# Kernel optimization log

Hardware: AMD Instinct MI355X
Metric: run time of the kernel (lower is better)

The kernel has to match this reference:

```python
import jax, jax.numpy as jnp
import numpy as np
import math

B, S, D = 1, 4096, 2048
H, KVH, HD = 32, 8, 64
W = 512            # sliding window size (== block size)
THETA = 10000.0
EPS = 1e-5
INTER = 5632
PRE_SCALE = 1.0 / math.sqrt(2.0)


def setup_inputs() -> dict:
    key = jax.random.key(0)
    ks = jax.random.split(key, 8)
    def w(k, shape, fan_in):
        return jax.random.normal(k, shape, jnp.float32) * (fan_in ** -0.5)
    return {
        "hidden_states": jax.random.normal(ks[0], (B, S, D), jnp.float32),
        "mixer_norm_w": jnp.ones((D,), jnp.float32),
        "wq": w(ks[1], (D, H * HD), D),
        "wk": w(ks[2], (D, KVH * HD), D),
        "wv": w(ks[3], (D, KVH * HD), D),
        "wo": w(ks[4], (H * HD, D), H * HD),
        "mlp_norm_w": jnp.ones((D,), jnp.float32),
        "w_gate": w(ks[5], (D, 2 * INTER), D),
        "w_down": w(ks[6], (INTER, D), INTER),
    }


def rmsnorm(x, w, eps=EPS):
    return x * jax.lax.rsqrt(jnp.mean(x * x, axis=-1, keepdims=True) + eps) * w


def rope(x):
    # x: [B, S, h, HD]; rotate-half RoPE
    half = HD // 2
    inv_freq = 1.0 / (THETA ** (jnp.arange(0, HD, 2, dtype=jnp.float32) / HD))
    freqs = jnp.arange(S, dtype=jnp.float32)[:, None] * inv_freq[None, :]  # [S, half]
    cos = jnp.cos(freqs)[None, :, None, :]
    sin = jnp.sin(freqs)[None, :, None, :]
    x1, x2 = x[..., :half], x[..., half:]
    return jnp.concatenate([x1 * cos - x2 * sin, x2 * cos + x1 * sin], axis=-1)


def sliding_attention(x, wq, wk, wv, wo):
    # x already pre-scaled; returns attn output (pre /pre_scale)
    q = (x @ wq).reshape(B, S, H, HD)
    k = (x @ wk).reshape(B, S, KVH, HD)
    v = (x @ wv).reshape(B, S, KVH, HD)
    q, k = rope(q), rope(k)
    rep = H // KVH
    k = jnp.repeat(k, rep, axis=2)  # [B,S,H,HD]
    v = jnp.repeat(v, rep, axis=2)
    nb = S // W
    qb = q.reshape(B, nb, W, H, HD)
    kb = k.reshape(B, nb, W, H, HD)
    vb = v.reshape(B, nb, W, H, HD)
    zeros = jnp.zeros((B, 1, W, H, HD), q.dtype)
    kw = jnp.concatenate([jnp.concatenate([zeros, kb[:, :-1]], axis=1), kb], axis=2)  # [B,nb,2W,H,HD]
    vw = jnp.concatenate([jnp.concatenate([zeros, vb[:, :-1]], axis=1), vb], axis=2)
    # local mask [nb, W, 2W]
    blk = jnp.arange(nb)[:, None, None]
    q_pos = blk * W + jnp.arange(W)[None, :, None]
    k_pos = blk * W - W + jnp.arange(2 * W)[None, None, :]
    mask = (k_pos >= 0) & (k_pos <= q_pos) & (q_pos - k_pos < W)
    scores = jnp.einsum("bnqhd,bnkhd->bhnqk", qb, kw) * (HD ** -0.5)
    scores = jnp.where(mask[None, None], scores, jnp.finfo(scores.dtype).min)
    p = jax.nn.softmax(scores, axis=-1)
    out = jnp.einsum("bhnqk,bnkhd->bnqhd", p, vw).reshape(B, S, H * HD)
    return out @ wo


def reference(hidden_states, mixer_norm_w, wq, wk, wv, wo, mlp_norm_w, w_gate, w_down):
    residual = hidden_states
    x = rmsnorm(hidden_states, mixer_norm_w)
    attn_out = sliding_attention(x * PRE_SCALE, wq, wk, wv, wo) / PRE_SCALE
    h = residual + attn_out
    xn = rmsnorm(h, mlp_norm_w)
    gv = xn @ w_gate
    gate, y = gv[..., :INTER], gv[..., INTER:]
    mlp_out = (jax.nn.silu(gate) * y) @ w_down
    return h + mlp_out
```

## Files before the change

kernel.cpp:

```cpp
#include <hip/hip_runtime.h>
#include <stdint.h>

typedef __attribute__((ext_vector_type(8))) short s16x8;
typedef __attribute__((ext_vector_type(4))) float f32x4;

#define GLD_LDS16(gp, lp) __builtin_amdgcn_global_load_lds( \
    (__attribute__((address_space(1))) void*)(void*)(gp), \
    (__attribute__((address_space(3))) void*)(lp), 16, 0, 0)

__device__ __forceinline__ float b2f(unsigned short s) {
    unsigned int u = ((unsigned int)s) << 16;
    return __builtin_bit_cast(float, u);
}
__device__ __forceinline__ unsigned short f2b(float f) {
    unsigned int u = __builtin_bit_cast(unsigned int, f);
    u = (u + 0x7FFFu + ((u >> 16) & 1u)) >> 16;
    return (unsigned short)u;
}
__device__ __forceinline__ f32x4 mfma16(s16x8 a, s16x8 b, f32x4 c) {
    return __builtin_amdgcn_mfma_f32_16x16x32_bf16(a, b, c, 0, 0, 0);
}
template <int N> __device__ __forceinline__ void waitvm() {
    if constexpr (N == 3) asm volatile("s_waitcnt vmcnt(3)" ::: "memory");
    else if constexpr (N == 4) asm volatile("s_waitcnt vmcnt(4)" ::: "memory");
}

__global__ __launch_bounds__(256) void rmsnorm_bf16(
    const float* __restrict__ x, const float* __restrict__ wgt,
    unsigned short* __restrict__ out)
{
    const int row = blockIdx.x;
    const int t = threadIdx.x;
    const float* xr = x + (size_t)row * 2048;
    float4 a = *(const float4*)(xr + t * 8);
    float4 b = *(const float4*)(xr + t * 8 + 4);
    float ss = a.x*a.x + a.y*a.y + a.z*a.z + a.w*a.w
             + b.x*b.x + b.y*b.y + b.z*b.z + b.w*b.w;
    #pragma unroll
    for (int d = 1; d < 64; d <<= 1) ss += __shfl_xor(ss, d);
    __shared__ float red[4];
    if ((t & 63) == 0) red[t >> 6] = ss;
    __syncthreads();
    float tot = red[0] + red[1] + red[2] + red[3];
    float inv = rsqrtf(tot * (1.0f / 2048.0f) + 1e-5f);
    float vals[8] = {a.x, a.y, a.z, a.w, b.x, b.y, b.z, b.w};
    const float* wr_ = wgt + t * 8;
    s16x8 ov;
    #pragma unroll
    for (int j = 0; j < 8; ++j) ov[j] = (short)f2b(vals[j] * inv * wr_[j]);
    *(s16x8*)(out + (size_t)row * 2048 + t * 8) = ov;
}

__global__ __launch_bounds__(256) void transpose_to_bf16(
    const float* __restrict__ in, unsigned short* __restrict__ out, int K, int N)
{
    __shared__ float tile[64][65];
    const int n0 = blockIdx.x * 64, k0 = blockIdx.y * 64;
    const int t = threadIdx.x;
    const int kr = t >> 4, nc = (t & 15) * 4;
    #pragma unroll
    for (int i = 0; i < 4; ++i) {
        float4 v = *(const float4*)(in + (size_t)(k0 + kr + i * 16) * N + n0 + nc);
        tile[nc + 0][kr + i * 16] = v.x;
        tile[nc + 1][kr + i * 16] = v.y;
        tile[nc + 2][kr + i * 16] = v.z;
        tile[nc + 3][kr + i * 16] = v.w;
    }
    __syncthreads();
    const int nr = t >> 3, kc = (t & 7) * 8;
    #pragma unroll
    for (int p = 0; p < 2; ++p) {
        s16x8 o;
        #pragma unroll
        for (int j = 0; j < 8; ++j) o[j] = (short)f2b(tile[nr + p * 32][kc + j]);
        *(s16x8*)(out + (size_t)(n0 + nr + p * 32) * K + k0 + kc) = o;
    }
}

template <int BN, int EPI>
__global__ __launch_bounds__(512, 2) void gemmq(
    const unsigned short* __restrict__ A,
    const unsigned short* __restrict__ B,
    void* __restrict__ Cv,
    const float* __restrict__ ADD,
    int N, int K)
{
    constexpr int WN  = BN / 4;
    constexpr int HN  = WN / 2;
    constexpr int NJQ = WN / 32;
    constexpr int NBU = BN / 64;
    constexpr int ABUF = 256 * 64;
    constexpr int BBUF = BN * 64;
    constexpr int W1   = 4;
    constexpr int W2   = (BN == 256) ? 4 : 3;
    constexpr int WEND = (BN == 256) ? 4 : 3;
    __shared__ __align__(16) unsigned short As[2 * ABUF];
    __shared__ __align__(16) unsigned short Bs[2 * BBUF];

    const int t = threadIdx.x;
    const int l = t & 63, w = t >> 6;
    const int l15 = l & 15, lg = l >> 4;
    const int wr = w >> 2, wc = w & 3;
    const int x7 = l15 & 7;
    const int cc0 = ((lg) ^ x7) << 3;
    const int cc1 = ((4 | lg) ^ x7) << 3;

    const int nwg = (int)gridDim.x;
    const int orig = (int)blockIdx.x;
    const int q8 = nwg >> 3, r8 = nwg & 7;
    const int xcd = orig & 7, lid = orig >> 3;
    const int wg = (xcd < r8 ? xcd * (q8 + 1) : r8 * (q8 + 1) + (xcd - r8) * q8) + lid;
    const int m0 = (wg & 15) * 256;
    const int n0 = (wg >> 4) * BN;

    const int tr = t >> 3;
    const int scol = ((t & 7) ^ (tr & 7)) << 3;
    const unsigned short* pA[4];
    #pragma unroll
    for (int u = 0; u < 4; ++u) {
        const int lrow = u * 64 + tr;
        const int g = ((lrow >> 6) & 1) * 128 + (lrow >> 7) * 64 + (lrow & 63);
        pA[u] = A + (size_t)(m0 + g) * K + scol;
    }
    const unsigned short* pB[NBU];
    #pragma unroll
    for (int u = 0; u < NBU; ++u) {
        const int lrow = u * 64 + tr;
        const int h = lrow / (BN / 2), rem = lrow % (BN / 2);
        const int g = (rem / HN) * WN + h * HN + (rem % HN);
        pB[u] = B + (size_t)(n0 + g) * K + scol;
    }

    f32x4 acc[2][2][4][NJQ] = {};
    s16x8 aF[4][2];
    s16x8 bF[2][NJQ][2];

    const int NT = K / 64;

    GLD_LDS16(pA[0], &As[0 * 4096 + t * 8]);
    GLD_LDS16(pA[1], &As[1 * 4096 + t * 8]);
    #pragma unroll
    for (int u = 0; u < NBU; ++u) GLD_LDS16(pB[u], &Bs[u * 4096 + t * 8]);
    GLD_LDS16(pA[2], &As[2 * 4096 + t * 8]);
    GLD_LDS16(pA[3], &As[3 * 4096 + t * 8]);
    waitvm<WEND>();
    __builtin_amdgcn_s_barrier();

    for (int kt = 0; kt < NT; ++kt) {
        const int rb  = (kt & 1) ? ABUF : 0;
        const int rbB = (kt & 1) ? BBUF : 0;
        const int wb  = ABUF - rb;
        const int wbB = BBUF - rbB;
        const int knext = (kt + 1 < NT ? kt + 1 : kt) * 64;

        #pragma unroll
        for (int i = 0; i < 4; ++i) {
            const int lr = wr * 64 + i * 16 + l15;
            aF[i][0] = *(const s16x8*)&As[rb + lr * 64 + cc0];
            aF[i][1] = *(const s16x8*)&As[rb + lr * 64 + cc1];
        }
        #pragma unroll
        for (int j = 0; j < NJQ; ++j) {
            const int lr = wc * HN + j * 16 + l15;
            bF[0][j][0] = *(const s16x8*)&Bs[rbB + lr * 64 + cc0];
            bF[0][j][1] = *(const s16x8*)&Bs[rbB + lr * 64 + cc1];
        }
        GLD_LDS16(pA[0] + knext, &As[wb + 0 * 4096 + t * 8]);
        GLD_LDS16(pA[1] + knext, &As[wb + 1 * 4096 + t * 8]);
        __builtin_amdgcn_s_barrier();
        __builtin_amdgcn_s_setprio(1);
        #pragma unroll
        for (int kk = 0; kk < 2; ++kk)
            #pragma unroll
            for (int i = 0; i < 4; ++i)
                #pragma unroll
                for (int j = 0; j < NJQ; ++j)
                    acc[0][0][i][j] = mfma16(aF[i][kk], bF[0][j][kk], acc[0][0][i][j]);
        __builtin_amdgcn_s_setprio(0);
        waitvm<W1>();
        __builtin_amdgcn_s_barrier();

        #pragma unroll
        for (int j = 0; j < NJQ; ++j) {
            const int lr = (BN / 2) + wc * HN + j * 16 + l15;
            bF[1][j][0] = *(const s16x8*)&Bs[rbB + lr * 64 + cc0];
            bF[1][j][1] = *(const s16x8*)&Bs[rbB + lr * 64 + cc1];
        }
        #pragma unroll
        for (int u = 0; u < NBU / 2; ++u)
            GLD_LDS16(pB[u] + knext, &Bs[wbB + u * 4096 + t * 8]);
        __builtin_amdgcn_s_barrier();
        __builtin_amdgcn_s_setprio(1);
        #pragma unroll
        for (int kk = 0; kk < 2; ++kk)
            #pragma unroll
            for (int i = 0; i < 4; ++i)
                #pragma unroll
                for (int j = 0; j < NJQ; ++j)
                    acc[0][1][i][j] = mfma16(aF[i][kk], bF[1][j][kk], acc[0][1][i][j]);
        __builtin_amdgcn_s_setprio(0);
        waitvm<W2>();
        __builtin_amdgcn_s_barrier();

        #pragma unroll
        for (int i = 0; i < 4; ++i) {
            const int lr = 128 + wr * 64 + i * 16 + l15;
            aF[i][0] = *(const s16x8*)&As[rb + lr * 64 + cc0];
            aF[i][1] = *(const s16x8*)&As[rb + lr * 64 + cc1];
        }
        #pragma unroll
        for (int u = NBU / 2; u < NBU; ++u)
            GLD_LDS16(pB[u] + knext, &Bs[wbB + u * 4096 + t * 8]);
        __builtin_amdgcn_s_barrier();
        __builtin_amdgcn_s_setprio(1);
        #pragma unroll
        for (int kk = 0; kk < 2; ++kk)
            #pragma unroll
            for (int i = 0; i < 4; ++i)
                #pragma unroll
                for (int j = 0; j < NJQ; ++j)
                    acc[1][0][i][j] = mfma16(aF[i][kk], bF[0][j][kk], acc[1][0][i][j]);
        __builtin_amdgcn_s_setprio(0);
        __builtin_amdgcn_s_barrier();

        GLD_LDS16(pA[2] + knext, &As[wb + 2 * 4096 + t * 8]);
        GLD_LDS16(pA[3] + knext, &As[wb + 3 * 4096 + t * 8]);
        __builtin_amdgcn_s_barrier();
        __builtin_amdgcn_s_setprio(1);
        #pragma unroll
        for (int kk = 0; kk < 2; ++kk)
            #pragma unroll
            for (int i = 0; i < 4; ++i)
                #pragma unroll
                for (int j = 0; j < NJQ; ++j)
                    acc[1][1][i][j] = mfma16(aF[i][kk], bF[1][j][kk], acc[1][1][i][j]);
        __builtin_amdgcn_s_setprio(0);
        waitvm<WEND>();
        __builtin_amdgcn_s_barrier();
    }

    #pragma unroll
    for (int qm = 0; qm < 2; ++qm)
        #pragma unroll
        for (int i = 0; i < 4; ++i)
            #pragma unroll
            for (int r = 0; r < 4; ++r) {
                const int row = m0 + wr * 128 + qm * 64 + i * 16 + lg * 4 + r;
                const size_t rbase = (size_t)row * N;
                #pragma unroll
                for (int qn = 0; qn < 2; ++qn)
                    #pragma unroll
                    for (int j = 0; j < NJQ; ++j) {
                        const int col = n0 + wc * WN + qn * HN + j * 16 + l15;
                        float v = acc[qm][qn][i][j][r];
                        if constexpr (EPI == 0) {
                            ((unsigned short*)Cv)[rbase + col] = f2b(v);
                        } else {
                            ((float*)Cv)[rbase + col] = v + ADD[rbase + col];
                        }
                    }
            }
}

__global__ __launch_bounds__(512, 2) void gemm_glu(
    const unsigned short* __restrict__ A,
    const unsigned short* __restrict__ Bg,
    const unsigned short* __restrict__ By,
    unsigned short* __restrict__ act,
    int N, int K)
{
    constexpr int ABUF = 256 * 64, BBUF = 128 * 64;
    __shared__ __align__(16) unsigned short As[2 * ABUF];
    __shared__ __align__(16) unsigned short Bgs[2 * BBUF];
    __shared__ __align__(16) unsigned short Bys[2 * BBUF];

    const int t = threadIdx.x;
    const int l = t & 63, w = t >> 6;
    const int l15 = l & 15, lg = l >> 4;
    const int wr = w >> 2, wc = w & 3;
    const int x7 = l15 & 7;
    const int cc0 = ((lg) ^ x7) << 3;
    const int cc1 = ((4 | lg) ^ x7) << 3;

    const int nwg = (int)gridDim.x;
    const int orig = (int)blockIdx.x;
    const int q8 = nwg >> 3;
    const int xcd = orig & 7, lid = orig >> 3;
    const int wg = xcd * q8 + lid;
    const int m0 = (wg & 15) * 256;
    const int n0 = (wg >> 4) * 128;

    const int tr = t >> 3;
    const int scol = ((t & 7) ^ (tr & 7)) << 3;
    const unsigned short* pA[4];
    #pragma unroll
    for (int u = 0; u < 4; ++u) {
        const int lrow = u * 64 + tr;
        const int g = ((lrow >> 6) & 1) * 128 + (lrow >> 7) * 64 + (lrow & 63);
        pA[u] = A + (size_t)(m0 + g) * K + scol;
    }
    const unsigned short *pG[2], *pY[2];
    #pragma unroll
    for (int u = 0; u < 2; ++u) {
        const int g = (tr >> 4) * 32 + u * 16 + (tr & 15);
        pG[u] = Bg + (size_t)(n0 + g) * K + scol;
        pY[u] = By + (size_t)(n0 + g) * K + scol;
    }

    f32x4 accG[2][2][4] = {};
    f32x4 accY[2][2][4] = {};
    s16x8 aF[4][2];
    s16x8 gF[2][2], yF[2][2];

    const int NT = K / 64;

    GLD_LDS16(pA[0], &As[0 * 4096 + t * 8]);
    GLD_LDS16(pA[1], &As[1 * 4096 + t * 8]);
    GLD_LDS16(pG[0], &Bgs[0 * 4096 + t * 8]);
    GLD_LDS16(pY[0], &Bys[0 * 4096 + t * 8]);
    GLD_LDS16(pG[1], &Bgs[1 * 4096 + t * 8]);
    GLD_LDS16(pY[1], &Bys[1 * 4096 + t * 8]);
    GLD_LDS16(pA[2], &As[2 * 4096 + t * 8]);
    GLD_LDS16(pA[3], &As[3 * 4096 + t * 8]);
    waitvm<4>();
    __builtin_amdgcn_s_barrier();

    for (int kt = 0; kt < NT; ++kt) {
        const int rb  = (kt & 1) ? ABUF : 0;
        const int rbB = (kt & 1) ? BBUF : 0;
        const int wb  = ABUF - rb;
        const int wbB = BBUF - rbB;
        const int knext = (kt + 1 < NT ? kt + 1 : kt) * 64;

        #pragma unroll
        for (int i = 0; i < 4; ++i) {
            const int lr = wr * 64 + i * 16 + l15;
            aF[i][0] = *(const s16x8*)&As[rb + lr * 64 + cc0];
            aF[i][1] = *(const s16x8*)&As[rb + lr * 64 + cc1];
        }
        {
            const int lr = wc * 16 + l15;
            gF[0][0] = *(const s16x8*)&Bgs[rbB + lr * 64 + cc0];
            gF[0][1] = *(const s16x8*)&Bgs[rbB + lr * 64 + cc1];
            yF[0][0] = *(const s16x8*)&Bys[rbB + lr * 64 + cc0];
            yF[0][1] = *(const s16x8*)&Bys[rbB + lr * 64 + cc1];
        }
        GLD_LDS16(pA[0] + knext, &As[wb + 0 * 4096 + t * 8]);
        GLD_LDS16(pA[1] + knext, &As[wb + 1 * 4096 + t * 8]);
        __builtin_amdgcn_s_barrier();
        __builtin_amdgcn_s_setprio(1);
        #pragma unroll
        for (int kk = 0; kk < 2; ++kk)
            #pragma unroll
            for (int i = 0; i < 4; ++i) {
                accG[0][0][i] = mfma16(aF[i][kk], gF[0][kk], accG[0][0][i]);
                accY[0][0][i] = mfma16(aF[i][kk], yF[0][kk], accY[0][0][i]);
            }
        __builtin_amdgcn_s_setprio(0);
        waitvm<4>();
        __builtin_amdgcn_s_barrier();

        {
            const int lr = 64 + wc * 16 + l15;
            gF[1][0] = *(const s16x8*)&Bgs[rbB + lr * 64 + cc0];
            gF[1][1] = *(const s16x8*)&Bgs[rbB + lr * 64 + cc1];
            yF[1][0] = *(const s16x8*)&Bys[rbB + lr * 64 + cc0];
            yF[1][1] = *(const s16x8*)&Bys[rbB + lr * 64 + cc1];
        }
        GLD_LDS16(pG[0] + knext, &Bgs[wbB + 0 * 4096 + t * 8]);
        GLD_LDS16(pY[0] + knext, &Bys[wbB + 0 * 4096 + t * 8]);
        __builtin_amdgcn_s_barrier();
        __builtin_amdgcn_s_setprio(1);
        #pragma unroll
        for (int kk = 0; kk < 2; ++kk)
            #pragma unroll
            for (int i = 0; i < 4; ++i) {
                accG[0][1][i] = mfma16(aF[i][kk], gF[1][kk], accG[0][1][i]);
                accY[0][1][i] = mfma16(aF[i][kk], yF[1][kk], accY[0][1][i]);
            }
        __builtin_amdgcn_s_setprio(0);
        waitvm<4>();
        __builtin_amdgcn_s_barrier();

        #pragma unroll
        for (int i = 0; i < 4; ++i) {
            const int lr = 128 + wr * 64 + i * 16 + l15;
            aF[i][0] = *(const s16x8*)&As[rb + lr * 64 + cc0];
            aF[i][1] = *(const s16x8*)&As[rb + lr * 64 + cc1];
        }
        GLD_LDS16(pG[1] + knext, &Bgs[wbB + 1 * 4096 + t * 8]);
        GLD_LDS16(pY[1] + knext, &Bys[wbB + 1 * 4096 + t * 8]);
        __builtin_amdgcn_s_barrier();
        __builtin_amdgcn_s_setprio(1);
        #pragma unroll
        for (int kk = 0; kk < 2; ++kk)
            #pragma unroll
            for (int i = 0; i < 4; ++i) {
                accG[1][0][i] = mfma16(aF[i][kk], gF[0][kk], accG[1][0][i]);
                accY[1][0][i] = mfma16(aF[i][kk], yF[0][kk], accY[1][0][i]);
            }
        __builtin_amdgcn_s_setprio(0);
        __builtin_amdgcn_s_barrier();

        GLD_LDS16(pA[2] + knext, &As[wb + 2 * 4096 + t * 8]);
        GLD_LDS16(pA[3] + knext, &As[wb + 3 * 4096 + t * 8]);
        __builtin_amdgcn_s_barrier();
        __builtin_amdgcn_s_setprio(1);
        #pragma unroll
        for (int kk = 0; kk < 2; ++kk)
            #pragma unroll
            for (int i = 0; i < 4; ++i) {
                accG[1][1][i] = mfma16(aF[i][kk], gF[1][kk], accG[1][1][i]);
                accY[1][1][i] = mfma16(aF[i][kk], yF[1][kk], accY[1][1][i]);
            }
        __builtin_amdgcn_s_setprio(0);
        waitvm<4>();
        __builtin_amdgcn_s_barrier();
    }

    #pragma unroll
    for (int qm = 0; qm < 2; ++qm)
        #pragma unroll
        for (int i = 0; i < 4; ++i)
            #pragma unroll
            for (int r = 0; r < 4; ++r) {
                const int row = m0 + wr * 128 + qm * 64 + i * 16 + lg * 4 + r;
                const size_t rbase = (size_t)row * N;
                #pragma unroll
                for (int qn = 0; qn < 2; ++qn) {
                    const int col = n0 + wc * 32 + qn * 16 + l15;
                    float g = accG[qm][qn][i][r];
                    float y = accY[qm][qn][i][r];
                    float sg = g / (1.0f + expf(-g));
                    act[rbase + col] = f2b(sg * y);
                }
            }
}

__global__ void rope_tab_k(float2* __restrict__ tab) {
    int i = blockIdx.x * 256 + threadIdx.x;
    if (i >= 4096 * 32) return;
    int s = i >> 5, d = i & 31;
    float inv = exp2f(-(float)d * (13.287712379549449f / 32.0f));
    float fr = (float)s * inv;
    float sv, cv;
    sincosf(fr, &sv, &cv);
    tab[i] = make_float2(cv, sv);
}

__global__ void rope_apply_k(unsigned short* __restrict__ qkv, const float2* __restrict__ tab) {
    int i = blockIdx.x * 256 + threadIdx.x;
    if (i >= 4096 * 40 * 4) return;
    int dg = i & 3;
    int rest = i >> 2;
    int head = rest % 40;
    int s = rest / 40;
    int off = head < 32 ? head * 64 : 2048 + (head - 32) * 64;
    unsigned short* p = qkv + (size_t)s * 3072 + off + dg * 8;
    s16x8 x1 = *(const s16x8*)p;
    s16x8 x2 = *(const s16x8*)(p + 32);
    const float2* tb = tab + s * 32 + dg * 8;
    s16x8 o1, o2;
    #pragma unroll
    for (int j = 0; j < 8; ++j) {
        float2 cs = tb[j];
        float a = b2f((unsigned short)x1[j]);
        float b = b2f((unsigned short)x2[j]);
        o1[j] = (short)f2b(a * cs.x - b * cs.y);
        o2[j] = (short)f2b(b * cs.x + a * cs.y);
    }
    *(s16x8*)p = o1;
    *(s16x8*)(p + 32) = o2;
}

__global__ __launch_bounds__(256) void attn_swa(
    const unsigned short* __restrict__ qkv,
    unsigned short* __restrict__ out)
{
    constexpr int LDQ = 3072;
    const int qb = blockIdx.x;
    const int h = blockIdx.y;
    const int kvh = h >> 2;
    const int q0 = qb * 64;
    const int t = threadIdx.x, l = t & 63, w = t >> 6;
    const int l15 = l & 15, lg = l >> 4;

    __shared__ unsigned short Kl[64 * 64];
    __shared__ unsigned short Vt[64 * 72];
    __shared__ unsigned short Pl[4 * 16 * 72];

    s16x8 qf[2];
    {
        const unsigned short* qp = qkv + (size_t)(q0 + w * 16 + l15) * LDQ + h * 64 + lg * 8;
        qf[0] = *(const s16x8*)(qp);
        qf[1] = *(const s16x8*)(qp + 32);
    }
    float m_run[4] = {-1e30f, -1e30f, -1e30f, -1e30f};
    float l_run[4] = {0.f, 0.f, 0.f, 0.f};
    f32x4 o[4] = {};

    const float SC = 0.0625f * 1.4426950408889634f;
    const int kt_lo = qb >= 8 ? qb - 8 : 0;

    for (int kt = kt_lo; kt <= qb; ++kt) {
        const int ks = kt * 64;
        __syncthreads();
        {
            const unsigned short* kg = qkv + (size_t)(ks + (t >> 3)) * LDQ + 2048 + kvh * 64 + (t & 7) * 8;
            GLD_LDS16(kg, Kl + t * 8);
            GLD_LDS16(kg + (size_t)32 * LDQ, Kl + t * 8 + 2048);
        }
        {
            const unsigned short* vg = qkv + (size_t)(ks + l) * LDQ + 2560 + kvh * 64 + w * 16;
            s16x8 v0 = *(const s16x8*)vg;
            s16x8 v1 = *(const s16x8*)(vg + 8);
            #pragma unroll
            for (int j = 0; j < 8; ++j) Vt[(w * 16 + j) * 72 + l] = (unsigned short)v0[j];
            #pragma unroll
            for (int j = 0; j < 8; ++j) Vt[(w * 16 + 8 + j) * 72 + l] = (unsigned short)v1[j];
        }
        __syncthreads();

        f32x4 sf[4] = {};
        #pragma unroll
        for (int kf = 0; kf < 4; ++kf) {
            #pragma unroll
            for (int kk = 0; kk < 2; ++kk) {
                s16x8 kb = *(const s16x8*)(Kl + (kf * 16 + l15) * 64 + kk * 32 + lg * 8);
                sf[kf] = mfma16(qf[kk], kb, sf[kf]);
            }
        }

        float tmax[4];
        #pragma unroll
        for (int r = 0; r < 4; ++r) {
            int qrow = q0 + w * 16 + lg * 4 + r;
            float mx = -1e30f;
            #pragma unroll
            for (int kf = 0; kf < 4; ++kf) {
                int key = ks + kf * 16 + l15;
                bool valid = (key <= qrow) && (qrow - key < 512);
                if (valid) mx = fmaxf(mx, sf[kf][r]);
            }
            #pragma unroll
            for (int d2 = 1; d2 < 16; d2 <<= 1) mx = fmaxf(mx, __shfl_xor(mx, d2));
            tmax[r] = mx;
        }

        float alpha[4], rsum[4];
        #pragma unroll
        for (int r = 0; r < 4; ++r) {
            float mnew = fmaxf(m_run[r], tmax[r]);
            alpha[r] = exp2f((m_run[r] - mnew) * SC);
            m_run[r] = mnew;
            rsum[r] = 0.f;
        }

        unsigned short* Pw = Pl + w * (16 * 72);
        #pragma unroll
        for (int kf = 0; kf < 4; ++kf) {
            #pragma unroll
            for (int r = 0; r < 4; ++r) {
                int qrow = q0 + w * 16 + lg * 4 + r;
                int key = ks + kf * 16 + l15;
                bool valid = (key <= qrow) && (qrow - key < 512);
                float p = valid ? exp2f((sf[kf][r] - m_run[r]) * SC) : 0.f;
                rsum[r] += p;
                Pw[(lg * 4 + r) * 72 + kf * 16 + l15] = f2b(p);
            }
        }
        #pragma unroll
        for (int r = 0; r < 4; ++r) {
            #pragma unroll
            for (int d2 = 1; d2 < 16; d2 <<= 1) rsum[r] += __shfl_xor(rsum[r], d2);
            l_run[r] = l_run[r] * alpha[r] + rsum[r];
        }
        #pragma unroll
        for (int hf = 0; hf < 4; ++hf)
            #pragma unroll
            for (int r = 0; r < 4; ++r) o[hf][r] *= alpha[r];

        asm volatile("s_waitcnt lgkmcnt(0)" ::: "memory");
        __builtin_amdgcn_sched_barrier(0);

        #pragma unroll
        for (int kk2 = 0; kk2 < 2; ++kk2) {
            s16x8 pa = *(const s16x8*)(Pw + l15 * 72 + kk2 * 32 + lg * 8);
            #pragma unroll
            for (int hf = 0; hf < 4; ++hf) {
                s16x8 vb = *(const s16x8*)(Vt + (hf * 16 + l15) * 72 + kk2 * 32 + lg * 8);
                o[hf] = mfma16(pa, vb, o[hf]);
            }
        }
    }

    #pragma unroll
    for (int r = 0; r < 4; ++r) {
        int qrow = q0 + w * 16 + lg * 4 + r;
        float invl = 1.0f / l_run[r];
        unsigned short* orow = out + (size_t)qrow * 2048 + h * 64;
        #pragma unroll
        for (int hf = 0; hf < 4; ++hf)
            orow[hf * 16 + l15] = f2b(o[hf][r] * invl);
    }
}

extern "C" void kernel_launch(void* const* d_in, const int* in_sizes, int n_in,
                              void* d_out, int out_size, void* d_ws, size_t ws_size,
                              hipStream_t stream)
{
    const float* hidden = (const float*)d_in[0];
    const float* w_mix  = (const float*)d_in[1];
    const float* wq     = (const float*)d_in[2];
    const float* wk     = (const float*)d_in[3];
    const float* wv     = (const float*)d_in[4];
    const float* wo     = (const float*)d_in[5];
    const float* w_mlp  = (const float*)d_in[6];
    const float* wg     = (const float*)d_in[7];
    const float* wd     = (const float*)d_in[8];
    float* out = (float*)d_out;

    char* ws = (char*)d_ws;
    size_t off = 0;
    auto alloc = [&](size_t bytes) {
        char* p = ws + off;
        off += (bytes + 255) & ~(size_t)255;
        return p;
    };
    unsigned short* Wt   = (unsigned short*)alloc((size_t)11264 * 2048 * 2);
    unsigned short* xn   = (unsigned short*)alloc((size_t)4096 * 2048 * 2);
    unsigned short* qkv  = (unsigned short*)alloc((size_t)4096 * 3072 * 2);
    float2*         rtab = (float2*)alloc((size_t)4096 * 32 * 8);
    unsigned short* attn = (unsigned short*)alloc((size_t)4096 * 2048 * 2);
    float*          hbuf = (float*)alloc((size_t)4096 * 2048 * 4);
    unsigned short* act  = (unsigned short*)alloc((size_t)4096 * 5632 * 2);

    rmsnorm_bf16<<<4096, 256, 0, stream>>>(hidden, w_mix, xn);

    transpose_to_bf16<<<dim3(32, 32), 256, 0, stream>>>(wq, Wt, 2048, 2048);
    transpose_to_bf16<<<dim3(8, 32), 256, 0, stream>>>(wk, Wt + (size_t)2048 * 2048, 2048, 512);
    transpose_to_bf16<<<dim3(8, 32), 256, 0, stream>>>(wv, Wt + (size_t)2560 * 2048, 2048, 512);

    gemmq<256, 0><<<192, 512, 0, stream>>>(xn, Wt, qkv, nullptr, 3072, 2048);

    rope_tab_k<<<(4096 * 32 + 255) / 256, 256, 0, stream>>>(rtab);
    rope_apply_k<<<(4096 * 40 * 4 + 255) / 256, 256, 0, stream>>>(qkv, rtab);

    attn_swa<<<dim3(64, 32), 256, 0, stream>>>(qkv, attn);

    transpose_to_bf16<<<dim3(32, 32), 256, 0, stream>>>(wo, Wt, 2048, 2048);
    gemmq<128, 1><<<256, 512, 0, stream>>>(attn, Wt, hbuf, hidden, 2048, 2048);

    rmsnorm_bf16<<<4096, 256, 0, stream>>>(hbuf, w_mlp, xn);

    transpose_to_bf16<<<dim3(176, 32), 256, 0, stream>>>(wg, Wt, 2048, 11264);
    gemm_glu<<<704, 512, 0, stream>>>(xn, Wt, Wt + (size_t)5632 * 2048, act, 5632, 2048);

    transpose_to_bf16<<<dim3(32, 88), 256, 0, stream>>>(wd, Wt, 5632, 2048);
    gemmq<128, 1><<<256, 512, 0, stream>>>(act, Wt, out, hbuf, 2048, 5632);
}
```

Before: 550.4 us.

## Collapse GEMM K-loop into single barrier per iteration with bulk prefetch

```diff
diff --git a/kernel.cpp b/kernel.cpp
--- a/kernel.cpp
+++ b/kernel.cpp
@@ -19,10 +19,6 @@
 }
 __device__ __forceinline__ f32x4 mfma16(s16x8 a, s16x8 b, f32x4 c) {
     return __builtin_amdgcn_mfma_f32_16x16x32_bf16(a, b, c, 0, 0, 0);
-}
-template <int N> __device__ __forceinline__ void waitvm() {
-    if constexpr (N == 3) asm volatile("s_waitcnt vmcnt(3)" ::: "memory");
-    else if constexpr (N == 4) asm volatile("s_waitcnt vmcnt(4)" ::: "memory");
 }
 
 __global__ __launch_bounds__(256) void rmsnorm_bf16(
@@ -91,9 +87,6 @@
     constexpr int NBU = BN / 64;
     constexpr int ABUF = 256 * 64;
     constexpr int BBUF = BN * 64;
-    constexpr int W1   = 4;
-    constexpr int W2   = (BN == 256) ? 4 : 3;
-    constexpr int WEND = (BN == 256) ? 4 : 3;
     __shared__ __align__(16) unsigned short As[2 * ABUF];
     __shared__ __align__(16) unsigned short Bs[2 * BBUF];
 
@@ -137,13 +130,11 @@
 
     const int NT = K / 64;
 
-    GLD_LDS16(pA[0], &As[0 * 4096 + t * 8]);
-    GLD_LDS16(pA[1], &As[1 * 4096 + t * 8]);
+    #pragma unroll
+    for (int u = 0; u < 4; ++u) GLD_LDS16(pA[u], &As[u * 4096 + t * 8]);
     #pragma unroll
     for (int u = 0; u < NBU; ++u) GLD_LDS16(pB[u], &Bs[u * 4096 + t * 8]);
-    GLD_LDS16(pA[2], &As[2 * 4096 + t * 8]);
-    GLD_LDS16(pA[3], &As[3 * 4096 + t * 8]);
-    waitvm<WEND>();
+    asm volatile("s_waitcnt vmcnt(0)" ::: "memory");
     __builtin_amdgcn_s_barrier();
 
     for (int kt = 0; kt < NT; ++kt) {
@@ -165,9 +156,9 @@
             bF[0][j][0] = *(const s16x8*)&Bs[rbB + lr * 64 + cc0];
             bF[0][j][1] = *(const s16x8*)&Bs[rbB + lr * 64 + cc1];
         }
-        GLD_LDS16(pA[0] + knext, &As[wb + 0 * 4096 + t * 8]);
-        GLD_LDS16(pA[1] + knext, &As[wb + 1 * 4096 + t * 8]);
-        __builtin_amdgcn_s_barrier();
+        #pragma unroll
+        for (int u = 0; u < 4; ++u)
+            GLD_LDS16(pA[u] + knext, &As[wb + u * 4096 + t * 8]);
         __builtin_amdgcn_s_setprio(1);
         #pragma unroll
         for (int kk = 0; kk < 2; ++kk)
@@ -177,8 +168,6 @@
                 for (int j = 0; j < NJQ; ++j)
                     acc[0][0][i][j] = mfma16(aF[i][kk], bF[0][j][kk], acc[0][0][i][j]);
         __builtin_amdgcn_s_setprio(0);
-        waitvm<W1>();
-        __builtin_amdgcn_s_barrier();
 
         #pragma unroll
         for (int j = 0; j < NJQ; ++j) {
@@ -187,9 +176,8 @@
             bF[1][j][1] = *(const s16x8*)&Bs[rbB + lr * 64 + cc1];
         }
         #pragma unroll
-        for (int u = 0; u < NBU / 2; ++u)
+        for (int u = 0; u < NBU; ++u)
             GLD_LDS16(pB[u] + knext, &Bs[wbB + u * 4096 + t * 8]);
-        __builtin_amdgcn_s_barrier();
         __builtin_amdgcn_s_setprio(1);
         #pragma unroll
         for (int kk = 0; kk < 2; ++kk)
@@ -199,8 +187,6 @@
                 for (int j = 0; j < NJQ; ++j)
                     acc[0][1][i][j] = mfma16(aF[i][kk], bF[1][j][kk], acc[0][1][i][j]);
         __builtin_amdgcn_s_setprio(0);
-        waitvm<W2>();
-        __builtin_amdgcn_s_barrier();
 
         #pragma unroll
         for (int i = 0; i < 4; ++i) {
@@ -208,10 +194,6 @@
             aF[i][0] = *(const s16x8*)&As[rb + lr * 64 + cc0];
             aF[i][1] = *(const s16x8*)&As[rb + lr * 64 + cc1];
         }
-        #pragma unroll
-        for (int u = NBU / 2; u < NBU; ++u)
-            GLD_LDS16(pB[u] + knext, &Bs[wbB + u * 4096 + t * 8]);
-        __builtin_amdgcn_s_barrier();
         __builtin_amdgcn_s_setprio(1);
         #pragma unroll
         for (int kk = 0; kk < 2; ++kk)
@@ -221,11 +203,7 @@
                 for (int j = 0; j < NJQ; ++j)
                     acc[1][0][i][j] = mfma16(aF[i][kk], bF[0][j][kk], acc[1][0][i][j]);
         __builtin_amdgcn_s_setprio(0);
-        __builtin_amdgcn_s_barrier();
-
-        GLD_LDS16(pA[2] + knext, &As[wb + 2 * 4096 + t * 8]);
-        GLD_LDS16(pA[3] + knext, &As[wb + 3 * 4096 + t * 8]);
-        __builtin_amdgcn_s_barrier();
+
         __builtin_amdgcn_s_setprio(1);
         #pragma unroll
         for (int kk = 0; kk < 2; ++kk)
@@ -235,7 +213,8 @@
                 for (int j = 0; j < NJQ; ++j)
                     acc[1][1][i][j] = mfma16(aF[i][kk], bF[1][j][kk], acc[1][1][i][j]);
         __builtin_amdgcn_s_setprio(0);
-        waitvm<WEND>();
+
+        asm volatile("s_waitcnt vmcnt(0)" ::: "memory");
         __builtin_amdgcn_s_barrier();
     }
 
@@ -314,15 +293,13 @@
 
     const int NT = K / 64;
 
-    GLD_LDS16(pA[0], &As[0 * 4096 + t * 8]);
-    GLD_LDS16(pA[1], &As[1 * 4096 + t * 8]);
+    #pragma unroll
+    for (int u = 0; u < 4; ++u) GLD_LDS16(pA[u], &As[u * 4096 + t * 8]);
     GLD_LDS16(pG[0], &Bgs[0 * 4096 + t * 8]);
     GLD_LDS16(pY[0], &Bys[0 * 4096 + t * 8]);
     GLD_LDS16(pG[1], &Bgs[1 * 4096 + t * 8]);
     GLD_LDS16(pY[1], &Bys[1 * 4096 + t * 8]);
-    GLD_LDS16(pA[2], &As[2 * 4096 + t * 8]);
-    GLD_LDS16(pA[3], &As[3 * 4096 + t * 8]);
-    waitvm<4>();
+    asm volatile("s_waitcnt vmcnt(0)" ::: "memory");
     __builtin_amdgcn_s_barrier();
 
     for (int kt = 0; kt < NT; ++kt) {
@@ -345,9 +322,9 @@
             yF[0][0] = *(const s16x8*)&Bys[rbB + lr * 64 + cc0];
             yF[0][1] = *(const s16x8*)&Bys[rbB + lr * 64 + cc1];
         }
-        GLD_LDS16(pA[0] + knext, &As[wb + 0 * 4096 + t * 8]);
-        GLD_LDS16(pA[1] + knext, &As[wb + 1 * 4096 + t * 8]);
-        __builtin_amdgcn_s_barrier();
+        #pragma unroll
+        for (int u = 0; u < 4; ++u)
+            GLD_LDS16(pA[u] + knext, &As[wb + u * 4096 + t * 8]);
         __builtin_amdgcn_s_setprio(1);
         #pragma unroll
         for (int kk = 0; kk < 2; ++kk)
@@ -357,8 +334,6 @@
                 accY[0][0][i] = mfma16(aF[i][kk], yF[0][kk], accY[0][0][i]);
             }
         __builtin_amdgcn_s_setprio(0);
-        waitvm<4>();
-        __builtin_amdgcn_s_barrier();
 
         {
             const int lr = 64 + wc * 16 + l15;
@@ -369,7 +344,8 @@
         }
         GLD_LDS16(pG[0] + knext, &Bgs[wbB + 0 * 4096 + t * 8]);
         GLD_LDS16(pY[0] + knext, &Bys[wbB + 0 * 4096 + t * 8]);
-        __builtin_amdgcn_s_barrier();
+        GLD_LDS16(pG[1] + knext, &Bgs[wbB + 1 * 4096 + t * 8]);
+        GLD_LDS16(pY[1] + knext, &Bys[wbB + 1 * 4096 + t * 8]);
         __builtin_amdgcn_s_setprio(1);
         #pragma unroll
         for (int kk = 0; kk < 2; ++kk)
@@ -379,8 +355,6 @@
                 accY[0][1][i] = mfma16(aF[i][kk], yF[1][kk], accY[0][1][i]);
             }
         __builtin_amdgcn_s_setprio(0);
-        waitvm<4>();
-        __builtin_amdgcn_s_barrier();
 
         #pragma unroll
         for (int i = 0; i < 4; ++i) {
@@ -388,9 +362,6 @@
             aF[i][0] = *(const s16x8*)&As[rb + lr * 64 + cc0];
             aF[i][1] = *(const s16x8*)&As[rb + lr * 64 + cc1];
         }
-        GLD_LDS16(pG[1] + knext, &Bgs[wbB + 1 * 4096 + t * 8]);
-        GLD_LDS16(pY[1] + knext, &Bys[wbB + 1 * 4096 + t * 8]);
-        __builtin_amdgcn_s_barrier();
         __builtin_amdgcn_s_setprio(1);
         #pragma unroll
         for (int kk = 0; kk < 2; ++kk)
@@ -400,11 +371,7 @@
                 accY[1][0][i] = mfma16(aF[i][kk], yF[0][kk], accY[1][0][i]);
             }
         __builtin_amdgcn_s_setprio(0);
-        __builtin_amdgcn_s_barrier();
-
-        GLD_LDS16(pA[2] + knext, &As[wb + 2 * 4096 + t * 8]);
-        GLD_LDS16(pA[3] + knext, &As[wb + 3 * 4096 + t * 8]);
-        __builtin_amdgcn_s_barrier();
+
         __builtin_amdgcn_s_setprio(1);
         #pragma unroll
         for (int kk = 0; kk < 2; ++kk)
@@ -414,7 +381,8 @@
                 accY[1][1][i] = mfma16(aF[i][kk], yF[1][kk], accY[1][1][i]);
             }
         __builtin_amdgcn_s_setprio(0);
-        waitvm<4>();
+
+        asm volatile("s_waitcnt vmcnt(0)" ::: "memory");
         __builtin_amdgcn_s_barrier();
     }
 
```

Measured after the change: 534.1 us. 3.0% less time.
